# Optimization experiments

Measured on AMD Instinct MI355X. Metric: run time of the kernel, lower is better.

## Reference

```python
import jax, jax.numpy as jnp
import numpy as np

B, L, H, VS = 128, 256, 128, 256  # vs = max(vocab_size, 2*H) = 256
THRESH = 0.4
EPS_NORM = 1e-12  # F.normalize eps
EPS_LN = 1e-5     # LayerNorm eps


def setup_inputs() -> dict:
    key = jax.random.key(0)
    ks = jax.random.split(key, 8)
    s = 0.02
    return {
        "seq": jax.random.randint(ks[0], (B, L), 0, VS),
        "embed": jax.random.normal(ks[1], (VS, H), dtype=jnp.float32) * s,
        "W1": jax.random.normal(ks[2], (2 * H, H), dtype=jnp.float32) * s,
        "b1": jnp.zeros((2 * H,), dtype=jnp.float32),
        "W2": jax.random.normal(ks[3], (H, 2 * H), dtype=jnp.float32) * s,
        "b2": jnp.zeros((H,), dtype=jnp.float32),
        "gamma": jnp.ones((H,), dtype=jnp.float32),
        "beta": jnp.zeros((H,), dtype=jnp.float32),
        "Wk": jax.random.normal(ks[4], (H, H), dtype=jnp.float32) * s,
        "Wr": jax.random.normal(ks[5], (H, H), dtype=jnp.float32) * s,
        "br": jnp.zeros((H,), dtype=jnp.float32),
        "Wo": jax.random.normal(ks[6], (VS, H), dtype=jnp.float32) * s,
        "bo": jnp.zeros((VS,), dtype=jnp.float32),
    }


def reference(seq, embed, W1, b1, W2, b2, gamma, beta, Wk, Wr, br, Wo, bo):
    # Embedding + FFN residual + LayerNorm
    h = embed[seq]                                    # (B,L,H)
    f = jax.nn.relu(h @ W1.T + b1) @ W2.T + b2        # (B,L,H)
    x = h + f
    mu = x.mean(-1, keepdims=True)
    var = x.var(-1, keepdims=True)                    # biased, matches torch LN
    h = (x - mu) / jnp.sqrt(var + EPS_LN) * gamma + beta

    # Precompute all keys, then sequential gated delta-rule update of M.
    K = h @ Wk.T                                      # (B,L,H), kp has no bias
    Kt = jnp.swapaxes(K, 0, 1)                        # (L,B,H)

    def step(M, k):                                   # M: (B,H,H), k: (B,H)
        kn = k / jnp.maximum(jnp.linalg.norm(k, axis=-1, keepdims=True), EPS_NORM)
        vp = jnp.einsum('bij,bj->bi', M, kn)          # predicted value
        err = k - vp
        d = err[:, :, None] * kn[:, None, :]          # outer-product write (B,H,H)
        # 'rel_norm' criterion: ||k - vp|| >= thresh * ||k||
        energy = jnp.linalg.norm(err, axis=-1)
        ref = THRESH * jnp.linalg.norm(k, axis=-1)
        g = (energy >= ref).astype(M.dtype)[:, None, None]
        return M + g * d, None

    M0 = jnp.zeros((B, H, H), dtype=h.dtype)
    M, _ = jax.lax.scan(step, M0, Kt[:-1])            # L-1 sequential steps

    q = Kt[-1]                                        # query from last position
    read = jnp.einsum('bij,bj->bi', M, q)             # (B,H)
    return (read @ Wr.T + br) @ Wo.T + bo             # (B,VS)
```

## Files before the change

### kernel.cpp

```cpp
#include <hip/hip_runtime.h>
#include <math.h>

#define B_   128
#define L_   256
#define H_   128
#define H2_  256
#define VS_  256
#define TOK_ (B_ * L_)

__device__ __forceinline__ float fma4(float4 a, float4 b, float acc) {
    acc = fmaf(a.x, b.x, acc);
    acc = fmaf(a.y, b.y, acc);
    acc = fmaf(a.z, b.z, acc);
    acc = fmaf(a.w, b.w, acc);
    return acc;
}

template <int CTRL>
__device__ __forceinline__ float dpp_add(float x) {
    int y = __builtin_amdgcn_update_dpp(0, __float_as_int(x), CTRL, 0xf, 0xf, true);
    return x + __int_as_float(y);
}
__device__ __forceinline__ float wave_sum(float x) {
    x = dpp_add<0x111>(x);
    x = dpp_add<0x112>(x);
    x = dpp_add<0x114>(x);
    x = dpp_add<0x118>(x);
    x = dpp_add<0x142>(x);
    x = dpp_add<0x143>(x);
    return x;
}
__device__ __forceinline__ float quad_sum(float x) {
    x = dpp_add<0xB1>(x);
    x = dpp_add<0x4E>(x);
    return x;
}

__global__ __launch_bounds__(256) void k_vffn(
    const float* __restrict__ embed,
    const float* __restrict__ W1, const float* __restrict__ b1,
    const float* __restrict__ W2, const float* __restrict__ b2,
    const float* __restrict__ gamma, const float* __restrict__ beta,
    const float* __restrict__ Wk, float* __restrict__ Fout)
{
    __shared__ float sh_h[4][128];
    __shared__ float sh_y[4][256];

    const int tid  = threadIdx.x;
    const int lane = tid & 63;
    const int r    = tid >> 6;
    const int v    = blockIdx.x * 4 + r;

    const float4* embed4 = (const float4*)embed;
    const float4* W1_4   = (const float4*)W1;
    const float4* W2_4   = (const float4*)W2;
    const float4* Wk_4   = (const float4*)Wk;

    if (lane < 32)
        *(float4*)&sh_h[r][lane * 4] = embed4[v * 32 + lane];
    __syncthreads();

    #pragma unroll
    for (int jj = 0; jj < 4; ++jj) {
        int j = jj * 64 + lane;
        const float4* wrow = W1_4 + j * 32;
        float acc = 0.f;
        #pragma unroll
        for (int c4 = 0; c4 < 32; ++c4)
            acc = fma4(*(const float4*)&sh_h[r][c4 * 4], wrow[c4], acc);
        sh_y[r][j] = fmaxf(acc + b1[j], 0.f);
    }
    __syncthreads();

    float xv[4];
    #pragma unroll
    for (int cc = 0; cc < 4; ++cc) {
        int c  = cc * 32 + (lane & 31);
        int hf = lane >> 5;
        const float4* wrow = W2_4 + c * 64 + hf * 32;
        float acc = 0.f;
        #pragma unroll
        for (int j4 = 0; j4 < 32; ++j4)
            acc = fma4(*(const float4*)&sh_y[r][(hf * 32 + j4) * 4], wrow[j4], acc);
        acc += __shfl_xor(acc, 32);
        xv[cc] = acc;
    }
    if (lane < 32) {
        #pragma unroll
        for (int cc = 0; cc < 4; ++cc) {
            int c = cc * 32 + lane;
            sh_h[r][c] = sh_h[r][c] + xv[cc] + b2[c];
        }
    }
    __syncthreads();

    {
        float2 x2 = *(const float2*)&sh_h[r][lane * 2];
        float s  = x2.x + x2.y;
        float s2 = x2.x * x2.x + x2.y * x2.y;
        s  += __shfl_xor(s, 1);  s  += __shfl_xor(s, 2);  s  += __shfl_xor(s, 4);
        s  += __shfl_xor(s, 8);  s  += __shfl_xor(s, 16); s  += __shfl_xor(s, 32);
        s2 += __shfl_xor(s2, 1); s2 += __shfl_xor(s2, 2); s2 += __shfl_xor(s2, 4);
        s2 += __shfl_xor(s2, 8); s2 += __shfl_xor(s2, 16); s2 += __shfl_xor(s2, 32);
        float mu   = s * (1.f / 128.f);
        float var  = s2 * (1.f / 128.f) - mu * mu;
        float rstd = 1.f / sqrtf(var + 1e-5f);
        float2 g2  = *(const float2*)&gamma[lane * 2];
        float2 be2 = *(const float2*)&beta[lane * 2];
        float2 o;
        o.x = (x2.x - mu) * rstd * g2.x + be2.x;
        o.y = (x2.y - mu) * rstd * g2.y + be2.y;
        *(float2*)&sh_h[r][lane * 2] = o;
    }
    __syncthreads();

    #pragma unroll
    for (int kk = 0; kk < 2; ++kk) {
        int k = kk * 64 + lane;
        const float4* wrow = Wk_4 + k * 32;
        float acc = 0.f;
        #pragma unroll
        for (int c4 = 0; c4 < 32; ++c4)
            acc = fma4(*(const float4*)&sh_h[r][c4 * 4], wrow[c4], acc);
        Fout[v * 128 + k] = acc;
    }
}

__global__ __launch_bounds__(512) void k_scan(
    const int* __restrict__ seq, const float* __restrict__ Fbuf,
    float* __restrict__ readout)
{
    extern __shared__ float smem_f[];
    float4* shk4  = (float4*)smem_f;
    float*  shkf  = smem_f;
    float*  rna   = smem_f + 32768;
    float*  thr   = rna + 256;
    float*  d01   = thr + 256;
    float*  red_f = d01 + 256;

    const int tid  = threadIdx.x;
    const int lane = tid & 63;
    const int w    = tid >> 6;
    const int cq   = lane & 3;
    const int row  = w * 16 + (lane >> 2);
    const int b    = blockIdx.x;
    const float4* F4 = (const float4*)Fbuf;
    const int* seqb = seq + b * 256;

    for (int f = tid; f < 8192; f += 512) {
        int t = f >> 5, c = f & 31;
        shk4[f] = F4[(size_t)seqb[t] * 32 + c];
    }
    __syncthreads();

    {
        int rr = tid >> 4, cc = tid & 15;
        for (int it = 0; it < 8; ++it) {
            int t  = it * 32 + rr;
            int tn = (t < 255) ? t + 1 : 255;
            float4 a0 = shk4[t  * 32 + cc], a1 = shk4[t  * 32 + 16 + cc];
            float4 b0 = shk4[tn * 32 + cc], b1 = shk4[tn * 32 + 16 + cc];
            float n2p = fma4(a1, a1, fma4(a0, a0, 0.f));
            float cp  = fma4(a1, b1, fma4(a0, b0, 0.f));
            n2p += __shfl_xor(n2p, 1); n2p += __shfl_xor(n2p, 2);
            n2p += __shfl_xor(n2p, 4); n2p += __shfl_xor(n2p, 8);
            cp  += __shfl_xor(cp, 1);  cp  += __shfl_xor(cp, 2);
            cp  += __shfl_xor(cp, 4);  cp  += __shfl_xor(cp, 8);
            if (cc == 0) {
                rna[t] = 1.f / fmaxf(sqrtf(n2p), 1e-12f);
                thr[t] = 0.16f * n2p;
                d01[t] = cp;
            }
        }
    }

    float4 m[8];
    #pragma unroll
    for (int u = 0; u < 8; ++u) m[u] = make_float4(0.f, 0.f, 0.f, 0.f);

    float4 kbE[8], kbO[8];
    {
        const float4* ks0 = shk4 + cq * 8;
        const float4* ks1 = shk4 + 32 + cq * 8;
        #pragma unroll
        for (int u = 0; u < 8; ++u) {
            kbE[u] = ks0[(u + cq) & 7];
            kbO[u] = ks1[(u + cq) & 7];
        }
    }
    float errR = shkf[row];
    {
        float e2p = (cq == 0) ? errR * errR : 0.f;
        e2p = wave_sum(e2p);
        if (lane == 63) red_f[w] = e2p;
    }
    __syncthreads();

#define REGION(T, KU, KM)                                                       \
  {                                                                             \
    const int t_ = (T);                                                         \
    float rnaT = rna[t_], rnaN = rna[t_ + 1];                                   \
    float thrT = thr[t_], d01T = d01[t_];                                       \
    float kselfN = shkf[(t_ + 1) * 128 + row];                                  \
    float4 ra = ((const float4*)red_f)[(t_ & 1) * 2];                           \
    float4 rb = ((const float4*)red_f)[(t_ & 1) * 2 + 1];                       \
               \
    float pA = 0.f, pB = 0.f;                                                   \
    pA = fma4(m[0], KM[0], pA); pB = fma4(m[1], KM[1], pB);                     \
    pA = fma4(m[2], KM[2], pA); pB = fma4(m[3], KM[3], pB);                     \
    pA = fma4(m[4], KM[4], pA); pB = fma4(m[5], KM[5], pB);                     \
    pA = fma4(m[6], KM[6], pA); pB = fma4(m[7], KM[7], pB);                     \
    float preM = quad_sum(pA + pB);                                             \
    float E2 = ((ra.x + ra.y) + (ra.z + ra.w)) +                                \
               ((rb.x + rb.y) + (rb.z + rb.w));                                 \
    float a_ = (E2 >= thrT) ? rnaT * errR : 0.f;                                \
    float pre = fmaf(a_, d01T, preM);               \
    float errN = fmaf(-rnaN, pre, kselfN);                                      \
            \
    float e2p = errN * errN;                                                    \
    e2p = dpp_add<0x114>(e2p);                                  \
    e2p = dpp_add<0x118>(e2p);                                  \
    e2p = dpp_add<0x142>(e2p);                                \
    e2p = dpp_add<0x143>(e2p);                \
    if (lane == 63) red_f[((t_ + 1) & 1) * 8 + w] = e2p;                        \
    __builtin_amdgcn_sched_barrier(0);                                          \
        \
    _Pragma("unroll")                                                           \
    for (int u = 0; u < 8; ++u) {                                               \
      m[u].x = fmaf(a_, KU[u].x, m[u].x);                                       \
      m[u].y = fmaf(a_, KU[u].y, m[u].y);                                       \
      m[u].z = fmaf(a_, KU[u].z, m[u].z);                                       \
      m[u].w = fmaf(a_, KU[u].w, m[u].w);                                       \
    }                                                                           \
    {                                                                           \
      const float4* ks = shk4 + (t_ + 2) * 32 + cq * 8;                         \
      _Pragma("unroll")                                                         \
      for (int u = 0; u < 8; ++u) KU[u] = ks[(u + cq) & 7];                     \
    }                                                                           \
    __builtin_amdgcn_sched_barrier(0);                                          \
                        \
    asm volatile("s_waitcnt lgkmcnt(8)" ::: "memory");                          \
    __builtin_amdgcn_sched_barrier(0);                                          \
    __builtin_amdgcn_s_barrier();                                               \
    errR = errN;                                                                \
  }

    for (int tt = 0; tt < 254; tt += 2) {
        REGION(tt,     kbE, kbO);
        REGION(tt + 1, kbO, kbE);
    }
#undef REGION

    {
        float4 ra = ((const float4*)red_f)[0];
        float4 rb = ((const float4*)red_f)[1];
        float E2 = ((ra.x + ra.y) + (ra.z + ra.w)) +
                   ((rb.x + rb.y) + (rb.z + rb.w));
        float a_ = (E2 >= thr[254]) ? rna[254] * errR : 0.f;
        float pA = 0.f, pB = 0.f;
        pA = fma4(m[0], kbO[0], pA); pB = fma4(m[1], kbO[1], pB);
        pA = fma4(m[2], kbO[2], pA); pB = fma4(m[3], kbO[3], pB);
        pA = fma4(m[4], kbO[4], pA); pB = fma4(m[5], kbO[5], pB);
        pA = fma4(m[6], kbO[6], pA); pB = fma4(m[7], kbO[7], pB);
        float preM = quad_sum(pA + pB);
        float pre  = fmaf(a_, d01[254], preM);
        if (cq == 0) readout[b * 128 + row] = pre;
    }
}

__global__ __launch_bounds__(256) void k_out(
    const float* __restrict__ readout,
    const float* __restrict__ Wr, const float* __restrict__ br,
    const float* __restrict__ Wo, const float* __restrict__ bo,
    float* __restrict__ out)
{
    __shared__ float sh_rd[128];
    __shared__ float sh_r2[128];
    const int b = blockIdx.x, tid = threadIdx.x;

    if (tid < 32) ((float4*)sh_rd)[tid] = ((const float4*)readout)[b * 32 + tid];
    __syncthreads();

    {
        int i = tid >> 1, h = tid & 1;
        const float4* Wr4 = (const float4*)Wr;
        const float4* rd4 = (const float4*)sh_rd;
        float s = 0.f;
        #pragma unroll
        for (int u = 0; u < 16; ++u) s = fma4(rd4[h * 16 + u], Wr4[i * 32 + h * 16 + u], s);
        s += __shfl_xor(s, 1);
        if (h == 0) sh_r2[i] = s + br[i];
    }
    __syncthreads();

    {
        const float4* Wo4 = (const float4*)Wo;
        const float4* r24 = (const float4*)sh_r2;
        float acc = bo[tid];
        #pragma unroll
        for (int u = 0; u < 32; ++u) acc = fma4(r24[u], Wo4[tid * 32 + u], acc);
        out[b * 256 + tid] = acc;
    }
}

extern "C" void kernel_launch(void* const* d_in, const int* in_sizes, int n_in,
                              void* d_out, int out_size, void* d_ws, size_t ws_size,
                              hipStream_t stream) {
    const int*   seq   = (const int*)  d_in[0];
    const float* embed = (const float*)d_in[1];
    const float* W1    = (const float*)d_in[2];
    const float* b1    = (const float*)d_in[3];
    const float* W2    = (const float*)d_in[4];
    const float* b2    = (const float*)d_in[5];
    const float* gamma = (const float*)d_in[6];
    const float* beta  = (const float*)d_in[7];
    const float* Wk    = (const float*)d_in[8];
    const float* Wr    = (const float*)d_in[9];
    const float* br    = (const float*)d_in[10];
    const float* Wo    = (const float*)d_in[11];
    const float* bo    = (const float*)d_in[12];

    float* Fbuf    = (float*)d_ws;
    float* readout = Fbuf + (size_t)VS_ * H_;
    float* out     = (float*)d_out;

    const size_t scan_lds = 32768 * 4 + 3 * 256 * 4 + 16 * 4;

    k_vffn<<<VS_ / 4, 256, 0, stream>>>(embed, W1, b1, W2, b2, gamma, beta, Wk, Fbuf);
    k_scan<<<B_,      512, scan_lds, stream>>>(seq, Fbuf, readout);
    k_out <<<B_,      256, 0, stream>>>(readout, Wr, br, Wo, bo, out);
}
```

Baseline: 163.6 us.

## Fuse output projection into scan, restructure scan thread mapping and per-vocab norms

```diff
diff --git a/kernel.cpp b/kernel.cpp
--- a/kernel.cpp
+++ b/kernel.cpp
@@ -6,7 +6,6 @@
 #define H_   128
 #define H2_  256
 #define VS_  256
-#define TOK_ (B_ * L_)
 
 __device__ __forceinline__ float fma4(float4 a, float4 b, float acc) {
     acc = fmaf(a.x, b.x, acc);
@@ -30,18 +29,14 @@
     x = dpp_add<0x143>(x);
     return x;
 }
-__device__ __forceinline__ float quad_sum(float x) {
-    x = dpp_add<0xB1>(x);
-    x = dpp_add<0x4E>(x);
-    return x;
-}
 
 __global__ __launch_bounds__(256) void k_vffn(
     const float* __restrict__ embed,
     const float* __restrict__ W1, const float* __restrict__ b1,
     const float* __restrict__ W2, const float* __restrict__ b2,
     const float* __restrict__ gamma, const float* __restrict__ beta,
-    const float* __restrict__ Wk, float* __restrict__ Fout)
+    const float* __restrict__ Wk, float* __restrict__ Fout,
+    float* __restrict__ n2g, float* __restrict__ rnag, float* __restrict__ thrg)
 {
     __shared__ float sh_h[4][128];
     __shared__ float sh_y[4][256];
@@ -114,192 +109,188 @@
     }
     __syncthreads();
 
-    #pragma unroll
-    for (int kk = 0; kk < 2; ++kk) {
-        int k = kk * 64 + lane;
-        const float4* wrow = Wk_4 + k * 32;
-        float acc = 0.f;
-        #pragma unroll
-        for (int c4 = 0; c4 < 32; ++c4)
-            acc = fma4(*(const float4*)&sh_h[r][c4 * 4], wrow[c4], acc);
-        Fout[v * 128 + k] = acc;
+    float fk0, fk1;
+    {
+        int k0 = lane, k1 = 64 + lane;
+        const float4* w0 = Wk_4 + k0 * 32;
+        const float4* w1 = Wk_4 + k1 * 32;
+        float a0 = 0.f, a1 = 0.f;
+        #pragma unroll
+        for (int c4 = 0; c4 < 32; ++c4) {
+            float4 h4 = *(const float4*)&sh_h[r][c4 * 4];
+            a0 = fma4(h4, w0[c4], a0);
+            a1 = fma4(h4, w1[c4], a1);
+        }
+        Fout[v * 128 + lane]      = a0;
+        Fout[v * 128 + 64 + lane] = a1;
+        fk0 = a0; fk1 = a1;
+    }
+    {
+        float n2 = fmaf(fk0, fk0, fk1 * fk1);
+        n2 += __shfl_xor(n2, 1);  n2 += __shfl_xor(n2, 2);  n2 += __shfl_xor(n2, 4);
+        n2 += __shfl_xor(n2, 8);  n2 += __shfl_xor(n2, 16); n2 += __shfl_xor(n2, 32);
+        if (lane == 0) {
+            n2g[v]  = n2;
+            rnag[v] = 1.f / fmaxf(sqrtf(n2), 1e-12f);
+            thrg[v] = 0.16f * n2;
+        }
     }
 }
 
 __global__ __launch_bounds__(512) void k_scan(
     const int* __restrict__ seq, const float* __restrict__ Fbuf,
-    float* __restrict__ readout)
-{
-    extern __shared__ float smem_f[];
-    float4* shk4  = (float4*)smem_f;
-    float*  shkf  = smem_f;
-    float*  rna   = smem_f + 32768;
-    float*  thr   = rna + 256;
-    float*  d01   = thr + 256;
-    float*  red_f = d01 + 256;
-
-    const int tid  = threadIdx.x;
-    const int lane = tid & 63;
-    const int w    = tid >> 6;
-    const int cq   = lane & 3;
-    const int row  = w * 16 + (lane >> 2);
-    const int b    = blockIdx.x;
-    const float4* F4 = (const float4*)Fbuf;
-    const int* seqb = seq + b * 256;
-
-    for (int f = tid; f < 8192; f += 512) {
-        int t = f >> 5, c = f & 31;
-        shk4[f] = F4[(size_t)seqb[t] * 32 + c];
-    }
-    __syncthreads();
-
-    {
-        int rr = tid >> 4, cc = tid & 15;
-        for (int it = 0; it < 8; ++it) {
-            int t  = it * 32 + rr;
-            int tn = (t < 255) ? t + 1 : 255;
-            float4 a0 = shk4[t  * 32 + cc], a1 = shk4[t  * 32 + 16 + cc];
-            float4 b0 = shk4[tn * 32 + cc], b1 = shk4[tn * 32 + 16 + cc];
-            float n2p = fma4(a1, a1, fma4(a0, a0, 0.f));
-            float cp  = fma4(a1, b1, fma4(a0, b0, 0.f));
-            n2p += __shfl_xor(n2p, 1); n2p += __shfl_xor(n2p, 2);
-            n2p += __shfl_xor(n2p, 4); n2p += __shfl_xor(n2p, 8);
-            cp  += __shfl_xor(cp, 1);  cp  += __shfl_xor(cp, 2);
-            cp  += __shfl_xor(cp, 4);  cp  += __shfl_xor(cp, 8);
-            if (cc == 0) {
-                rna[t] = 1.f / fmaxf(sqrtf(n2p), 1e-12f);
-                thr[t] = 0.16f * n2p;
-                d01[t] = cp;
-            }
-        }
-    }
-
-    float4 m[8];
-    #pragma unroll
-    for (int u = 0; u < 8; ++u) m[u] = make_float4(0.f, 0.f, 0.f, 0.f);
-
-    float4 kbE[8], kbO[8];
-    {
-        const float4* ks0 = shk4 + cq * 8;
-        const float4* ks1 = shk4 + 32 + cq * 8;
-        #pragma unroll
-        for (int u = 0; u < 8; ++u) {
-            kbE[u] = ks0[(u + cq) & 7];
-            kbO[u] = ks1[(u + cq) & 7];
-        }
-    }
-    float errR = shkf[row];
-    {
-        float e2p = (cq == 0) ? errR * errR : 0.f;
-        e2p = wave_sum(e2p);
-        if (lane == 63) red_f[w] = e2p;
-    }
-    __syncthreads();
-
-#define REGION(T, KU, KM)                                                       \
-  {                                                                             \
-    const int t_ = (T);                                                         \
-    float rnaT = rna[t_], rnaN = rna[t_ + 1];                                   \
-    float thrT = thr[t_], d01T = d01[t_];                                       \
-    float kselfN = shkf[(t_ + 1) * 128 + row];                                  \
-    float4 ra = ((const float4*)red_f)[(t_ & 1) * 2];                           \
-    float4 rb = ((const float4*)red_f)[(t_ & 1) * 2 + 1];                       \
-               \
-    float pA = 0.f, pB = 0.f;                                                   \
-    pA = fma4(m[0], KM[0], pA); pB = fma4(m[1], KM[1], pB);                     \
-    pA = fma4(m[2], KM[2], pA); pB = fma4(m[3], KM[3], pB);                     \
-    pA = fma4(m[4], KM[4], pA); pB = fma4(m[5], KM[5], pB);                     \
-    pA = fma4(m[6], KM[6], pA); pB = fma4(m[7], KM[7], pB);                     \
-    float preM = quad_sum(pA + pB);                                             \
-    float E2 = ((ra.x + ra.y) + (ra.z + ra.w)) +                                \
-               ((rb.x + rb.y) + (rb.z + rb.w));                                 \
-    float a_ = (E2 >= thrT) ? rnaT * errR : 0.f;                                \
-    float pre = fmaf(a_, d01T, preM);               \
-    float errN = fmaf(-rnaN, pre, kselfN);                                      \
-            \
-    float e2p = errN * errN;                                                    \
-    e2p = dpp_add<0x114>(e2p);                                  \
-    e2p = dpp_add<0x118>(e2p);                                  \
-    e2p = dpp_add<0x142>(e2p);                                \
-    e2p = dpp_add<0x143>(e2p);                \
-    if (lane == 63) red_f[((t_ + 1) & 1) * 8 + w] = e2p;                        \
-    __builtin_amdgcn_sched_barrier(0);                                          \
-        \
-    _Pragma("unroll")                                                           \
-    for (int u = 0; u < 8; ++u) {                                               \
-      m[u].x = fmaf(a_, KU[u].x, m[u].x);                                       \
-      m[u].y = fmaf(a_, KU[u].y, m[u].y);                                       \
-      m[u].z = fmaf(a_, KU[u].z, m[u].z);                                       \
-      m[u].w = fmaf(a_, KU[u].w, m[u].w);                                       \
-    }                                                                           \
-    {                                                                           \
-      const float4* ks = shk4 + (t_ + 2) * 32 + cq * 8;                         \
-      _Pragma("unroll")                                                         \
-      for (int u = 0; u < 8; ++u) KU[u] = ks[(u + cq) & 7];                     \
-    }                                                                           \
-    __builtin_amdgcn_sched_barrier(0);                                          \
-                        \
-    asm volatile("s_waitcnt lgkmcnt(8)" ::: "memory");                          \
-    __builtin_amdgcn_sched_barrier(0);                                          \
-    __builtin_amdgcn_s_barrier();                                               \
-    errR = errN;                                                                \
-  }
-
-    for (int tt = 0; tt < 254; tt += 2) {
-        REGION(tt,     kbE, kbO);
-        REGION(tt + 1, kbO, kbE);
-    }
-#undef REGION
-
-    {
-        float4 ra = ((const float4*)red_f)[0];
-        float4 rb = ((const float4*)red_f)[1];
-        float E2 = ((ra.x + ra.y) + (ra.z + ra.w)) +
-                   ((rb.x + rb.y) + (rb.z + rb.w));
-        float a_ = (E2 >= thr[254]) ? rna[254] * errR : 0.f;
-        float pA = 0.f, pB = 0.f;
-        pA = fma4(m[0], kbO[0], pA); pB = fma4(m[1], kbO[1], pB);
-        pA = fma4(m[2], kbO[2], pA); pB = fma4(m[3], kbO[3], pB);
-        pA = fma4(m[4], kbO[4], pA); pB = fma4(m[5], kbO[5], pB);
-        pA = fma4(m[6], kbO[6], pA); pB = fma4(m[7], kbO[7], pB);
-        float preM = quad_sum(pA + pB);
-        float pre  = fmaf(a_, d01[254], preM);
-        if (cq == 0) readout[b * 128 + row] = pre;
-    }
-}
-
-__global__ __launch_bounds__(256) void k_out(
-    const float* __restrict__ readout,
+    const float* __restrict__ n2g, const float* __restrict__ rnag,
+    const float* __restrict__ thrg,
     const float* __restrict__ Wr, const float* __restrict__ br,
     const float* __restrict__ Wo, const float* __restrict__ bo,
     float* __restrict__ out)
 {
-    __shared__ float sh_rd[128];
-    __shared__ float sh_r2[128];
-    const int b = blockIdx.x, tid = threadIdx.x;
-
-    if (tid < 32) ((float4*)sh_rd)[tid] = ((const float4*)readout)[b * 32 + tid];
-    __syncthreads();
-
-    {
-        int i = tid >> 1, h = tid & 1;
+    __shared__ float part_[2][4][128];
+    __shared__ float red_[2][2];
+    __shared__ float rna_[256];
+    __shared__ float thr_[256];
+    __shared__ float d01_[256];
+    __shared__ int   seqb_[256];
+
+    const int tid  = threadIdx.x;
+    const int lane = tid & 63;
+    const int w    = tid >> 6;
+    const int cc   = w & 3;
+    const int rh   = w >> 2;
+    const int row  = rh * 64 + lane;
+    const int b    = blockIdx.x;
+    const float4* F4 = (const float4*)Fbuf;
+
+    if (tid < 256) seqb_[tid] = seq[b * 256 + tid];
+    __syncthreads();
+
+    if (tid < 256) {
+        int v = seqb_[tid];
+        rna_[tid] = rnag[v];
+        thr_[tid] = thrg[v];
+    } else if (tid < 511) {
+        int t = tid - 256;
+        int va = seqb_[t], vb = seqb_[t + 1];
+        const float4* A  = F4 + va * 32;
+        const float4* Bp = F4 + vb * 32;
+        float a0 = 0.f, a1 = 0.f, a2 = 0.f, a3 = 0.f;
+        #pragma unroll
+        for (int u = 0; u < 8; ++u) {
+            a0 = fma4(A[u],      Bp[u],      a0);
+            a1 = fma4(A[8 + u],  Bp[8 + u],  a1);
+            a2 = fma4(A[16 + u], Bp[16 + u], a2);
+            a3 = fma4(A[24 + u], Bp[24 + u], a3);
+        }
+        d01_[t] = (a0 + a1) + (a2 + a3);
+    }
+    part_[0][tid >> 7][tid & 127] = 0.f;
+    if (tid == 0) red_[0][1] = 0.f;
+    if (tid == 1) red_[0][0] = n2g[seqb_[0]];
+
+    float errT = Fbuf[(size_t)seqb_[0] * 128 + row];
+    float ksA  = Fbuf[(size_t)seqb_[1] * 128 + row];
+    float ksB  = 0.f;
+    float4 m[8], kb0[8], kb1[8], kb2[8];
+    {
+        int v0 = seqb_[0], v1 = seqb_[1], v2 = seqb_[2];
+        #pragma unroll
+        for (int u = 0; u < 8; ++u) {
+            m[u]   = make_float4(0.f, 0.f, 0.f, 0.f);
+            kb0[u] = F4[(size_t)v0 * 32 + cc * 8 + u];
+            kb1[u] = F4[(size_t)v1 * 32 + cc * 8 + u];
+            kb2[u] = F4[(size_t)v2 * 32 + cc * 8 + u];
+        }
+    }
+    __syncthreads();
+
+#define REG(T, BU, BM, KSU, KSP)                                                \
+  {                                                                             \
+    const int t_ = (T), pr = t_ & 1, pw = pr ^ 1;                               \
+    int sv2 = seqb_[t_ + 2];                                                    \
+    int sv3 = seqb_[(t_ + 3 > 255) ? 255 : t_ + 3];                             \
+    float p0 = part_[pr][0][row], p1 = part_[pr][1][row];                       \
+    float p2 = part_[pr][2][row], p3 = part_[pr][3][row];                       \
+    float r0 = red_[pr][0], r1 = red_[pr][1];                                   \
+    float rnaT = rna_[t_], thrT = thr_[t_], d01T = d01_[t_];                    \
+    float rnaN = rna_[t_ + 1];                                                  \
+    float praw = (p0 + p1) + (p2 + p3);                                         \
+    float E2 = r0 + r1;                                                         \
+    float av = (E2 >= thrT) ? rnaT * errT : 0.f;                                \
+    float pre = fmaf(av, d01T, praw);                \
+    float errN = fmaf(-rnaN, pre, KSU);                                         \
+    float e2p = wave_sum(errN * errN);                                          \
+    if (cc == 0 && lane == 63) red_[pw][rh] = e2p;                              \
+    KSP = Fbuf[(size_t)sv2 * 128 + row];                \
+    _Pragma("unroll")                                                           \
+    for (int u = 0; u < 8; ++u) {                          \
+      m[u].x = fmaf(av, BU[u].x, m[u].x);                                       \
+      m[u].y = fmaf(av, BU[u].y, m[u].y);                                       \
+      m[u].z = fmaf(av, BU[u].z, m[u].z);                                       \
+      m[u].w = fmaf(av, BU[u].w, m[u].w);                                       \
+    }                                                                           \
+    float q0 = 0.f, q1 = 0.f, q2 = 0.f, q3 = 0.f;                               \
+    q0 = fma4(m[0], BM[0], q0); q1 = fma4(m[1], BM[1], q1);                     \
+    q2 = fma4(m[2], BM[2], q2); q3 = fma4(m[3], BM[3], q3);                     \
+    q0 = fma4(m[4], BM[4], q0); q1 = fma4(m[5], BM[5], q1);                     \
+    q2 = fma4(m[6], BM[6], q2); q3 = fma4(m[7], BM[7], q3);                     \
+    part_[pw][cc][row] = (q0 + q1) + (q2 + q3);        \
+    _Pragma("unroll")                                                           \
+    for (int u = 0; u < 8; ++u)                \
+      BU[u] = F4[(size_t)sv3 * 32 + cc * 8 + u];                                \
+    __builtin_amdgcn_sched_barrier(0);                                          \
+    asm volatile("s_waitcnt lgkmcnt(0)" ::: "memory");                          \
+    __builtin_amdgcn_sched_barrier(0);                                          \
+    __builtin_amdgcn_s_barrier();                                               \
+    __builtin_amdgcn_sched_barrier(0);                                          \
+    errT = errN;                                                                \
+  }
+
+    for (int tt = 0; tt < 252; tt += 6) {
+        REG(tt + 0, kb0, kb2, ksA, ksB);
+        REG(tt + 1, kb1, kb0, ksB, ksA);
+        REG(tt + 2, kb2, kb1, ksA, ksB);
+        REG(tt + 3, kb0, kb2, ksB, ksA);
+        REG(tt + 4, kb1, kb0, ksA, ksB);
+        REG(tt + 5, kb2, kb1, ksB, ksA);
+    }
+    REG(252, kb0, kb2, ksA, ksB);
+    REG(253, kb1, kb0, ksB, ksA);
+#undef REG
+
+    float* rd_ = &part_[1][0][0];
+    float* r2_ = &part_[1][1][0];
+    {
+        float p0 = part_[0][0][row], p1 = part_[0][1][row];
+        float p2 = part_[0][2][row], p3 = part_[0][3][row];
+        float praw = (p0 + p1) + (p2 + p3);
+        float E2 = red_[0][0] + red_[0][1];
+        float av = (E2 >= thr_[254]) ? rna_[254] * errT : 0.f;
+        float pre = fmaf(av, d01_[254], praw);
+        if (cc == 0) rd_[row] = pre;
+    }
+    __syncthreads();
+
+    {
+        int i = tid >> 2, q = tid & 3;
         const float4* Wr4 = (const float4*)Wr;
-        const float4* rd4 = (const float4*)sh_rd;
+        const float4* rdv = (const float4*)rd_;
         float s = 0.f;
         #pragma unroll
-        for (int u = 0; u < 16; ++u) s = fma4(rd4[h * 16 + u], Wr4[i * 32 + h * 16 + u], s);
+        for (int u = 0; u < 8; ++u) s = fma4(rdv[q * 8 + u], Wr4[i * 32 + q * 8 + u], s);
         s += __shfl_xor(s, 1);
-        if (h == 0) sh_r2[i] = s + br[i];
-    }
-    __syncthreads();
-
-    {
+        s += __shfl_xor(s, 2);
+        if (q == 0) r2_[i] = s + br[i];
+    }
+    __syncthreads();
+    {
+        int v = tid >> 1, h = tid & 1;
         const float4* Wo4 = (const float4*)Wo;
-        const float4* r24 = (const float4*)sh_r2;
-        float acc = bo[tid];
-        #pragma unroll
-        for (int u = 0; u < 32; ++u) acc = fma4(r24[u], Wo4[tid * 32 + u], acc);
-        out[b * 256 + tid] = acc;
+        const float4* r2v = (const float4*)r2_;
+        float s = 0.f;
+        #pragma unroll
+        for (int u = 0; u < 16; ++u) s = fma4(r2v[h * 16 + u], Wo4[v * 32 + h * 16 + u], s);
+        s += __shfl_xor(s, 1);
+        if (h == 0) out[b * 256 + v] = s + bo[v];
     }
 }
 
@@ -320,13 +311,14 @@
     const float* Wo    = (const float*)d_in[11];
     const float* bo    = (const float*)d_in[12];
 
-    float* Fbuf    = (float*)d_ws;
-    float* readout = Fbuf + (size_t)VS_ * H_;
-    float* out     = (float*)d_out;
-
-    const size_t scan_lds = 32768 * 4 + 3 * 256 * 4 + 16 * 4;
-
-    k_vffn<<<VS_ / 4, 256, 0, stream>>>(embed, W1, b1, W2, b2, gamma, beta, Wk, Fbuf);
-    k_scan<<<B_,      512, scan_lds, stream>>>(seq, Fbuf, readout);
-    k_out <<<B_,      256, 0, stream>>>(readout, Wr, br, Wo, bo, out);
-}
+    float* Fbuf = (float*)d_ws;
+    float* n2g  = Fbuf + VS_ * H_;
+    float* rnag = n2g + VS_;
+    float* thrg = rnag + VS_;
+    float* out  = (float*)d_out;
+
+    k_vffn<<<VS_ / 4, 256, 0, stream>>>(embed, W1, b1, W2, b2, gamma, beta, Wk,
+                                        Fbuf, n2g, rnag, thrg);
+    k_scan<<<B_, 512, 0, stream>>>(seq, Fbuf, n2g, rnag, thrg,
+                                   Wr, br, Wo, bo, out);
+}
```

Measured after the change: 232.6 us. +42.2%, slower.
